# Optimization experiments

Hardware: AMD Instinct MI355X
Metric: run time of the kernel (lower is better)

## Reference

```python
import jax, jax.numpy as jnp
import numpy as np
import math

B, S, D, H = 4, 2048, 1024, 16
DH = D // H  # 64

def setup_inputs() -> dict:
    key = jax.random.key(0)
    ks = jax.random.split(key, 6)
    return {
        "x": jax.random.normal(ks[0], (B, S, D), dtype=jnp.float32),
        "alibi": jax.random.normal(ks[1], (1, H, S, S), dtype=jnp.float32),
        "w_qkv": jax.random.normal(ks[2], (3 * D, D), dtype=jnp.float32) * 0.02,
        "b_qkv": jax.random.normal(ks[3], (3 * D,), dtype=jnp.float32) * 0.02,
        "w_o": jax.random.normal(ks[4], (D, D), dtype=jnp.float32) * 0.02,
        "b_o": jax.random.normal(ks[5], (D,), dtype=jnp.float32) * 0.02,
    }

def reference(x, alibi, w_qkv, b_qkv, w_o, b_o):
    b, s, d = x.shape
    # torch Linear: y = x @ W.T + b
    qkv = x @ w_qkv.T + b_qkv                       # [B, S, 3D]
    qkv = qkv.reshape(b, s, H, 3, DH)               # interleaved per-head q,k,v
    q = jnp.swapaxes(qkv[:, :, :, 0, :], 1, 2)      # [B, H, S, DH]
    k = jnp.swapaxes(qkv[:, :, :, 1, :], 1, 2)
    v = jnp.swapaxes(qkv[:, :, :, 2, :], 1, 2)
    scores = jnp.einsum("bhqd,bhkd->bhqk", q, k) / math.sqrt(DH)
    attn = jax.nn.softmax(scores + alibi, axis=-1)  # [B, H, S, S]
    o = jnp.einsum("bhqk,bhkd->bhqd", attn, v)      # [B, H, S, DH]
    o = jnp.swapaxes(o, 1, 2).reshape(b, s, d)      # [B, S, D]
    return o @ w_o.T + b_o
```

## Files before the change

kernel.cpp:

```cpp
#include <hip/hip_runtime.h>
#include <stdint.h>

#define S_LEN 2048
#define NH    16
#define NB    4
#define DH    64
#define DMODEL 1024

using bf16x8 = __attribute__((ext_vector_type(8))) __bf16;
using f32x4  = __attribute__((ext_vector_type(4))) float;
using us8    = __attribute__((ext_vector_type(8))) unsigned short;

__device__ __forceinline__ unsigned short f2bf_rne(float f) {
    unsigned u = __builtin_bit_cast(unsigned, f);
    return (unsigned short)((u + 0x7FFFu + ((u >> 16) & 1u)) >> 16);
}

__device__ __forceinline__ bf16x8 ld_bf8(const unsigned short* p) {
    return __builtin_bit_cast(bf16x8, *(const us8*)p);
}

__device__ __forceinline__ f32x4 mfma16(bf16x8 a, bf16x8 b, f32x4 c) {
    return __builtin_amdgcn_mfma_f32_16x16x32_bf16(a, b, c, 0, 0, 0);
}

__device__ __forceinline__ float fast_exp2(float x) {
#if __has_builtin(__builtin_amdgcn_exp2f)
    return __builtin_amdgcn_exp2f(x);
#else
    return __expf(x * 0.69314718056f);
#endif
}

typedef __attribute__((address_space(1))) void* gp1_t;
typedef __attribute__((address_space(3))) void* lp3_t;

__device__ __forceinline__ void gload_lds16(const void* g, void* l) {
    __builtin_amdgcn_global_load_lds((gp1_t)(const_cast<void*>(g)), (lp3_t)l, 16, 0, 0);
}

__global__ void cvt_bf16(const float* __restrict__ in, unsigned short* __restrict__ out, int n4) {
    int i = blockIdx.x * 256 + threadIdx.x;
    if (i < n4) {
        float4 v = ((const float4*)in)[i];
        ushort4 o;
        o.x = f2bf_rne(v.x); o.y = f2bf_rne(v.y);
        o.z = f2bf_rne(v.z); o.w = f2bf_rne(v.w);
        ((ushort4*)out)[i] = o;
    }
}

template <int EPI>
__global__ __launch_bounds__(256) void gemm128(
    const unsigned short* __restrict__ A,
    const unsigned short* __restrict__ W,
    const float* __restrict__ bias,
    float* __restrict__ outF,
    unsigned short* __restrict__ Qb,
    unsigned short* __restrict__ Kb,
    unsigned short* __restrict__ Vt,
    int nTilesN)
{
    __shared__ __align__(16) unsigned short As[128 * 32];
    __shared__ __align__(16) unsigned short Bs[128 * 32];

    const int bm = blockIdx.x / nTilesN;
    const int bn = blockIdx.x % nTilesN;
    const int tileM = bm * 128, tileN = bn * 128;
    const int tid = threadIdx.x, lane = tid & 63, w = tid >> 6;
    const int m16 = lane & 15, quad = lane >> 4;
    const int wm = w >> 1, wn = w & 1;

    f32x4 acc[4][4] = {};

    const int c0 = w * 64 + lane;
    const int r0 = c0 >> 2, k0 = (c0 & 3) * 8;
    const int c1 = (4 + w) * 64 + lane;
    const int r1 = c1 >> 2, k1 = (c1 & 3) * 8;

    const unsigned short* Ag0 = A + (size_t)(tileM + r0) * 1024 + k0;
    const unsigned short* Ag1 = A + (size_t)(tileM + r1) * 1024 + k1;
    const unsigned short* Bg0 = W + (size_t)(tileN + r0) * 1024 + k0;
    const unsigned short* Bg1 = W + (size_t)(tileN + r1) * 1024 + k1;
    unsigned short* lA0 = &As[w * 512];
    unsigned short* lA1 = &As[(4 + w) * 512];
    unsigned short* lB0 = &Bs[w * 512];
    unsigned short* lB1 = &Bs[(4 + w) * 512];

    for (int kk = 0; kk < 1024; kk += 32) {
        gload_lds16(Ag0 + kk, lA0);
        gload_lds16(Ag1 + kk, lA1);
        gload_lds16(Bg0 + kk, lB0);
        gload_lds16(Bg1 + kk, lB1);
        __syncthreads();

        bf16x8 af[4], bf[4];
#pragma unroll
        for (int i = 0; i < 4; i++)
            af[i] = ld_bf8(&As[(wm * 64 + i * 16 + m16) * 32 + quad * 8]);
#pragma unroll
        for (int j = 0; j < 4; j++)
            bf[j] = ld_bf8(&Bs[(wn * 64 + j * 16 + m16) * 32 + quad * 8]);
#pragma unroll
        for (int i = 0; i < 4; i++)
#pragma unroll
            for (int j = 0; j < 4; j++)
                acc[i][j] = mfma16(af[i], bf[j], acc[i][j]);
        __syncthreads();
    }

#pragma unroll
    for (int i = 0; i < 4; i++) {
        const int mrow = tileM + wm * 64 + i * 16 + quad * 4;
#pragma unroll
        for (int j = 0; j < 4; j++) {
            const int nb0 = tileN + wn * 64 + j * 16;
            const int n = nb0 + m16;
            const float bv = bias[n];
            if (EPI == 0) {
                const int hh = nb0 / 192, rem = nb0 % 192;
                const int t = rem / 64, dbase = rem % 64;
                const int d = dbase + m16;
#pragma unroll
                for (int r = 0; r < 4; r++) {
                    float val = acc[i][j][r] + bv;
                    const int m = mrow + r;
                    const int b_ = m >> 11, s_ = m & 2047;
                    const size_t bh = (size_t)b_ * NH + hh;
                    if (t == 0)
                        Qb[(bh * S_LEN + s_) * DH + d] = f2bf_rne(val * 0.18033688f);
                    else if (t == 1)
                        Kb[(bh * S_LEN + s_) * DH + d] = f2bf_rne(val);
                    else
                        Vt[(bh * DH + d) * S_LEN + s_] = f2bf_rne(val);
                }
            } else {
#pragma unroll
                for (int r = 0; r < 4; r++) {
                    const int m = mrow + r;
                    outF[(size_t)m * DMODEL + n] = acc[i][j][r] + bv;
                }
            }
        }
    }
}

__global__ __launch_bounds__(256, 4) void attn(const unsigned short* __restrict__ Qb,
                                               const unsigned short* __restrict__ Kb,
                                               const unsigned short* __restrict__ Vt,
                                               const float* __restrict__ alibi,
                                               unsigned short* __restrict__ ob) {
    const int blk = blockIdx.x;
    const int xcd = blk & 7;
    const int b_  = (blk >> 3) & 3;
    const int hq  = xcd * 32 + (blk >> 5);
    const int hh  = hq >> 4, qt = hq & 15;
    const int tid = threadIdx.x, lane = tid & 63, w = tid >> 6;
    const int m16 = lane & 15, quad = lane >> 4;
    const int q0 = qt * 128;
    const size_t bh = (size_t)b_ * NH + hh;

    const unsigned short* Qp = Qb + (bh * S_LEN) * DH;
    const unsigned short* Kp = Kb + bh * S_LEN * DH;
    const unsigned short* Vp = Vt + bh * DH * S_LEN;

    __shared__ __align__(16) unsigned short Ks[128 * 64];
    __shared__ __align__(16) unsigned short Vs[64 * 128];
    __shared__ __align__(16) unsigned int   Pl[4][16 * 20];

    bf16x8 qfrag[2][2];
#pragma unroll
    for (int qf = 0; qf < 2; qf++) {
        const unsigned short* qp = Qp + (size_t)(q0 + w * 32 + qf * 16 + m16) * DH + quad * 8;
        qfrag[qf][0] = ld_bf8(qp);
        qfrag[qf][1] = ld_bf8(qp + 32);
    }
    const float* Apq[2];
#pragma unroll
    for (int qf = 0; qf < 2; qf++)
        Apq[qf] = alibi + ((size_t)hh * S_LEN + q0 + w * 32 + qf * 16 + m16) * S_LEN + quad * 4;

    int offk[4], offv[4];
#pragma unroll
    for (int t = 0; t < 4; t++) {
        const int ck = (w * 4 + t) * 64 + lane;
        const int rk = ck >> 3;
        offk[t] = rk * DH + ((ck & 7) ^ (rk & 7)) * 8;
        const int cv = ck;
        const int dv = cv >> 4;
        offv[t] = dv * S_LEN + ((cv & 15) ^ (dv & 15)) * 8;
    }

    const bf16x8 onesf = __builtin_bit_cast(bf16x8, (us8)(0x3F80u));
    f32x4 oacc[2][4] = {};
    f32x4 ssum[2] = {};
    unsigned int* plw = &Pl[w][0];
    const int sA = m16 & 7;

    for (int kc = 0; kc < S_LEN; kc += 128) {
        __syncthreads();
#pragma unroll
        for (int t = 0; t < 4; t++)
            gload_lds16(Kp + (size_t)kc * DH + offk[t], &Ks[(w * 4 + t) * 512]);
#pragma unroll
        for (int t = 0; t < 4; t++)
            gload_lds16(Vp + kc + offv[t], &Vs[(w * 4 + t) * 512]);
        __syncthreads();

#pragma unroll
        for (int qf = 0; qf < 2; qf++) {
            const bf16x8 qa = qfrag[qf][0], qb2 = qfrag[qf][1];
#pragma unroll
            for (int kc2 = 0; kc2 < 4; kc2++) {
                f32x4 sc[2];
#pragma unroll
                for (int t = 0; t < 2; t++) {
                    const int krow = (kc2 * 2 + t) * 16 + m16;
                    f32x4 z = {};
                    z = mfma16(ld_bf8(&Ks[krow * DH + (quad ^ sA) * 8]), qa, z);
                    z = mfma16(ld_bf8(&Ks[krow * DH + ((quad + 4) ^ sA) * 8]), qb2, z);
                    sc[t] = z;
                }
#pragma unroll
                for (int t = 0; t < 2; t++) {
                    const float4 al = *(const float4*)(Apq[qf] + kc + kc2 * 32 + t * 16);
                    float p0 = fast_exp2(__builtin_fmaf(al.x, 1.44269504f, sc[t][0]));
                    float p1 = fast_exp2(__builtin_fmaf(al.y, 1.44269504f, sc[t][1]));
                    float p2 = fast_exp2(__builtin_fmaf(al.z, 1.44269504f, sc[t][2]));
                    float p3 = fast_exp2(__builtin_fmaf(al.w, 1.44269504f, sc[t][3]));
                    uint2 pk;
                    pk.x = (__builtin_bit_cast(unsigned, p0) >> 16) |
                           (__builtin_bit_cast(unsigned, p1) & 0xFFFF0000u);
                    pk.y = (__builtin_bit_cast(unsigned, p2) >> 16) |
                           (__builtin_bit_cast(unsigned, p3) & 0xFFFF0000u);
                    *(uint2*)&plw[m16 * 20 + t * 8 + quad * 2] = pk;
                }
                const bf16x8 pf = ld_bf8((const unsigned short*)&plw[m16 * 20 + quad * 4]);
                ssum[qf] = mfma16(pf, onesf, ssum[qf]);
#pragma unroll
                for (int db = 0; db < 4; db++) {
                    const int vrow = db * 16 + m16;
                    const bf16x8 vf = ld_bf8(&Vs[vrow * 128 + ((kc2 * 4 + quad) ^ m16) * 8]);
                    oacc[qf][db] = mfma16(pf, vf, oacc[qf][db]);
                }
            }
        }
    }

#pragma unroll
    for (int qf = 0; qf < 2; qf++) {
        f32x4 rinv;
#pragma unroll
        for (int r = 0; r < 4; r++) rinv[r] = 1.0f / ssum[qf][r];
#pragma unroll
        for (int db = 0; db < 4; db++)
#pragma unroll
            for (int r = 0; r < 4; r++) {
                const int q = q0 + w * 32 + qf * 16 + quad * 4 + r;
                ob[((size_t)b_ * S_LEN + q) * DMODEL + hh * DH + db * 16 + m16] =
                    f2bf_rne(oacc[qf][db][r] * rinv[r]);
            }
    }
}

extern "C" void kernel_launch(void* const* d_in, const int* in_sizes, int n_in,
                              void* d_out, int out_size, void* d_ws, size_t ws_size,
                              hipStream_t stream) {
    (void)in_sizes; (void)n_in; (void)out_size; (void)ws_size;
    const float* x      = (const float*)d_in[0];
    const float* alibi  = (const float*)d_in[1];
    const float* w_qkv  = (const float*)d_in[2];
    const float* b_qkv  = (const float*)d_in[3];
    const float* w_o    = (const float*)d_in[4];
    const float* b_o    = (const float*)d_in[5];
    float* out = (float*)d_out;

    char* ws = (char*)d_ws;
    unsigned short* xb    = (unsigned short*)(ws);
    unsigned short* wqkvb = (unsigned short*)(ws + 16777216);
    unsigned short* wob   = (unsigned short*)(ws + 23068672);
    unsigned short* Qb    = (unsigned short*)(ws + 25165824);
    unsigned short* Kb    = (unsigned short*)(ws + 41943040);
    unsigned short* Vt    = (unsigned short*)(ws + 58720256);
    unsigned short* ob    = (unsigned short*)(ws + 75497472);

    cvt_bf16<<<8192, 256, 0, stream>>>(x, xb, 8388608 / 4);
    cvt_bf16<<<3072, 256, 0, stream>>>(w_qkv, wqkvb, 3145728 / 4);
    cvt_bf16<<<1024, 256, 0, stream>>>(w_o, wob, 1048576 / 4);

    gemm128<0><<<64 * 24, 256, 0, stream>>>(xb, wqkvb, b_qkv, nullptr, Qb, Kb, Vt, 24);
    attn<<<1024, 256, 0, stream>>>(Qb, Kb, Vt, alibi, ob);
    gemm128<1><<<64 * 8, 256, 0, stream>>>(ob, wob, b_o, out, nullptr, nullptr, nullptr, 8);
}
```

Before: 649.0 us.

## Rewrite attention inner loop with 32x32x16 MFMA and register-shuffled P

```diff
diff --git a/kernel.cpp b/kernel.cpp
--- a/kernel.cpp
+++ b/kernel.cpp
@@ -9,6 +9,7 @@
 
 using bf16x8 = __attribute__((ext_vector_type(8))) __bf16;
 using f32x4  = __attribute__((ext_vector_type(4))) float;
+using f32x16 = __attribute__((ext_vector_type(16))) float;
 using us8    = __attribute__((ext_vector_type(8))) unsigned short;
 
 __device__ __forceinline__ unsigned short f2bf_rne(float f) {
@@ -22,6 +23,10 @@
 
 __device__ __forceinline__ f32x4 mfma16(bf16x8 a, bf16x8 b, f32x4 c) {
     return __builtin_amdgcn_mfma_f32_16x16x32_bf16(a, b, c, 0, 0, 0);
+}
+
+__device__ __forceinline__ f32x16 mfma32(bf16x8 a, bf16x8 b, f32x16 c) {
+    return __builtin_amdgcn_mfma_f32_32x32x16_bf16(a, b, c, 0, 0, 0);
 }
 
 __device__ __forceinline__ float fast_exp2(float x) {
@@ -121,18 +126,23 @@
                 const int hh = nb0 / 192, rem = nb0 % 192;
                 const int t = rem / 64, dbase = rem % 64;
                 const int d = dbase + m16;
-#pragma unroll
-                for (int r = 0; r < 4; r++) {
-                    float val = acc[i][j][r] + bv;
-                    const int m = mrow + r;
-                    const int b_ = m >> 11, s_ = m & 2047;
-                    const size_t bh = (size_t)b_ * NH + hh;
-                    if (t == 0)
-                        Qb[(bh * S_LEN + s_) * DH + d] = f2bf_rne(val * 0.18033688f);
-                    else if (t == 1)
-                        Kb[(bh * S_LEN + s_) * DH + d] = f2bf_rne(val);
-                    else
-                        Vt[(bh * DH + d) * S_LEN + s_] = f2bf_rne(val);
+                const int b_ = mrow >> 11, s0 = mrow & 2047;
+                const size_t bh = (size_t)b_ * NH + hh;
+                if (t == 2) {
+                    ushort4 pk;
+                    pk.x = f2bf_rne(acc[i][j][0] + bv);
+                    pk.y = f2bf_rne(acc[i][j][1] + bv);
+                    pk.z = f2bf_rne(acc[i][j][2] + bv);
+                    pk.w = f2bf_rne(acc[i][j][3] + bv);
+                    *(ushort4*)&Vt[(bh * DH + d) * S_LEN + s0] = pk;
+                } else {
+#pragma unroll
+                    for (int r = 0; r < 4; r++) {
+                        float val = acc[i][j][r] + bv;
+                        const size_t idx = (bh * S_LEN + s0 + r) * DH + d;
+                        if (t == 0) Qb[idx] = f2bf_rne(val * 0.18033688f);
+                        else        Kb[idx] = f2bf_rne(val);
+                    }
                 }
             } else {
 #pragma unroll
@@ -151,116 +161,119 @@
                                                const float* __restrict__ alibi,
                                                unsigned short* __restrict__ ob) {
     const int blk = blockIdx.x;
-    const int xcd = blk & 7;
-    const int b_  = (blk >> 3) & 3;
-    const int hq  = xcd * 32 + (blk >> 5);
-    const int hh  = hq >> 4, qt = hq & 15;
+    const int xcd   = blk & 7;
+    const int inner = blk >> 3;
+    const int hh = (inner & 1) * 8 + xcd;
+    const int b_ = (inner >> 1) & 3;
+    const int qt = inner >> 3;
     const int tid = threadIdx.x, lane = tid & 63, w = tid >> 6;
-    const int m16 = lane & 15, quad = lane >> 4;
+    const int l31 = lane & 31, h = lane >> 5;
     const int q0 = qt * 128;
     const size_t bh = (size_t)b_ * NH + hh;
 
-    const unsigned short* Qp = Qb + (bh * S_LEN) * DH;
     const unsigned short* Kp = Kb + bh * S_LEN * DH;
     const unsigned short* Vp = Vt + bh * DH * S_LEN;
 
     __shared__ __align__(16) unsigned short Ks[128 * 64];
     __shared__ __align__(16) unsigned short Vs[64 * 128];
-    __shared__ __align__(16) unsigned int   Pl[4][16 * 20];
-
-    bf16x8 qfrag[2][2];
-#pragma unroll
-    for (int qf = 0; qf < 2; qf++) {
-        const unsigned short* qp = Qp + (size_t)(q0 + w * 32 + qf * 16 + m16) * DH + quad * 8;
-        qfrag[qf][0] = ld_bf8(qp);
-        qfrag[qf][1] = ld_bf8(qp + 32);
-    }
-    const float* Apq[2];
-#pragma unroll
-    for (int qf = 0; qf < 2; qf++)
-        Apq[qf] = alibi + ((size_t)hh * S_LEN + q0 + w * 32 + qf * 16 + m16) * S_LEN + quad * 4;
-
-    int offk[4], offv[4];
-#pragma unroll
-    for (int t = 0; t < 4; t++) {
-        const int ck = (w * 4 + t) * 64 + lane;
-        const int rk = ck >> 3;
-        offk[t] = rk * DH + ((ck & 7) ^ (rk & 7)) * 8;
-        const int cv = ck;
-        const int dv = cv >> 4;
-        offv[t] = dv * S_LEN + ((cv & 15) ^ (dv & 15)) * 8;
-    }
-
-    const bf16x8 onesf = __builtin_bit_cast(bf16x8, (us8)(0x3F80u));
-    f32x4 oacc[2][4] = {};
-    f32x4 ssum[2] = {};
-    unsigned int* plw = &Pl[w][0];
-    const int sA = m16 & 7;
+
+    const int qrow = q0 + w * 32 + l31;
+    bf16x8 qfrag[4];
+#pragma unroll
+    for (int kd = 0; kd < 4; kd++)
+        qfrag[kd] = ld_bf8(Qb + (bh * S_LEN + qrow) * DH + kd * 16 + h * 8);
+
+    const float* Ap = alibi + ((size_t)hh * S_LEN + qrow) * S_LEN + h * 4;
+
+    int koff[4], voff[4];
+#pragma unroll
+    for (int i = 0; i < 4; i++) {
+        const int u = i * 256 + w * 64 + lane;
+        const int kr = u >> 3, kc_ = u & 7;
+        koff[i] = kr * DH + (kc_ ^ (kr & 7)) * 8;
+        const int vd = u >> 4, vc = u & 15;
+        voff[i] = vd * S_LEN + (vc ^ (vd & 15)) * 8;
+    }
+
+    f32x16 oacc[2] = {};
+    float ssum = 0.0f;
 
     for (int kc = 0; kc < S_LEN; kc += 128) {
         __syncthreads();
 #pragma unroll
-        for (int t = 0; t < 4; t++)
-            gload_lds16(Kp + (size_t)kc * DH + offk[t], &Ks[(w * 4 + t) * 512]);
-#pragma unroll
-        for (int t = 0; t < 4; t++)
-            gload_lds16(Vp + kc + offv[t], &Vs[(w * 4 + t) * 512]);
+        for (int i = 0; i < 4; i++)
+            gload_lds16(Kp + (size_t)kc * DH + koff[i], &Ks[(i * 256 + w * 64) * 8]);
+#pragma unroll
+        for (int i = 0; i < 4; i++)
+            gload_lds16(Vp + kc + voff[i], &Vs[(i * 256 + w * 64) * 8]);
         __syncthreads();
 
 #pragma unroll
-        for (int qf = 0; qf < 2; qf++) {
-            const bf16x8 qa = qfrag[qf][0], qb2 = qfrag[qf][1];
-#pragma unroll
-            for (int kc2 = 0; kc2 < 4; kc2++) {
-                f32x4 sc[2];
-#pragma unroll
-                for (int t = 0; t < 2; t++) {
-                    const int krow = (kc2 * 2 + t) * 16 + m16;
-                    f32x4 z = {};
-                    z = mfma16(ld_bf8(&Ks[krow * DH + (quad ^ sA) * 8]), qa, z);
-                    z = mfma16(ld_bf8(&Ks[krow * DH + ((quad + 4) ^ sA) * 8]), qb2, z);
-                    sc[t] = z;
-                }
-#pragma unroll
-                for (int t = 0; t < 2; t++) {
-                    const float4 al = *(const float4*)(Apq[qf] + kc + kc2 * 32 + t * 16);
-                    float p0 = fast_exp2(__builtin_fmaf(al.x, 1.44269504f, sc[t][0]));
-                    float p1 = fast_exp2(__builtin_fmaf(al.y, 1.44269504f, sc[t][1]));
-                    float p2 = fast_exp2(__builtin_fmaf(al.z, 1.44269504f, sc[t][2]));
-                    float p3 = fast_exp2(__builtin_fmaf(al.w, 1.44269504f, sc[t][3]));
-                    uint2 pk;
-                    pk.x = (__builtin_bit_cast(unsigned, p0) >> 16) |
-                           (__builtin_bit_cast(unsigned, p1) & 0xFFFF0000u);
-                    pk.y = (__builtin_bit_cast(unsigned, p2) >> 16) |
-                           (__builtin_bit_cast(unsigned, p3) & 0xFFFF0000u);
-                    *(uint2*)&plw[m16 * 20 + t * 8 + quad * 2] = pk;
-                }
-                const bf16x8 pf = ld_bf8((const unsigned short*)&plw[m16 * 20 + quad * 4]);
-                ssum[qf] = mfma16(pf, onesf, ssum[qf]);
-#pragma unroll
-                for (int db = 0; db < 4; db++) {
-                    const int vrow = db * 16 + m16;
-                    const bf16x8 vf = ld_bf8(&Vs[vrow * 128 + ((kc2 * 4 + quad) ^ m16) * 8]);
-                    oacc[qf][db] = mfma16(pf, vf, oacc[qf][db]);
-                }
+        for (int kt = 0; kt < 4; kt++) {
+            f32x16 sacc = {};
+#pragma unroll
+            for (int kd = 0; kd < 4; kd++) {
+                const bf16x8 kf =
+                    ld_bf8(&Ks[(kt * 32 + l31) * DH + (((kd * 2 + h) ^ (l31 & 7)) * 8)]);
+                sacc = mfma32(kf, qfrag[kd], sacc);
+            }
+            unsigned Sd[8];
+#pragma unroll
+            for (int g = 0; g < 4; g++) {
+                const float4 al = *(const float4*)(Ap + kc + kt * 32 + g * 8);
+                unsigned u0 = __builtin_bit_cast(unsigned,
+                    fast_exp2(__builtin_fmaf(al.x, 1.44269504f, sacc[4 * g + 0]))) & 0xFFFF0000u;
+                unsigned u1 = __builtin_bit_cast(unsigned,
+                    fast_exp2(__builtin_fmaf(al.y, 1.44269504f, sacc[4 * g + 1]))) & 0xFFFF0000u;
+                unsigned u2 = __builtin_bit_cast(unsigned,
+                    fast_exp2(__builtin_fmaf(al.z, 1.44269504f, sacc[4 * g + 2]))) & 0xFFFF0000u;
+                unsigned u3 = __builtin_bit_cast(unsigned,
+                    fast_exp2(__builtin_fmaf(al.w, 1.44269504f, sacc[4 * g + 3]))) & 0xFFFF0000u;
+                ssum += (__builtin_bit_cast(float, u0) + __builtin_bit_cast(float, u1)) +
+                        (__builtin_bit_cast(float, u2) + __builtin_bit_cast(float, u3));
+                Sd[2 * g]     = (u0 >> 16) | u1;
+                Sd[2 * g + 1] = (u2 >> 16) | u3;
+            }
+            const unsigned r0 = (unsigned)__shfl_xor((int)(h ? Sd[0] : Sd[2]), 32);
+            const unsigned r1 = (unsigned)__shfl_xor((int)(h ? Sd[1] : Sd[3]), 32);
+            const unsigned r2 = (unsigned)__shfl_xor((int)(h ? Sd[4] : Sd[6]), 32);
+            const unsigned r3 = (unsigned)__shfl_xor((int)(h ? Sd[5] : Sd[7]), 32);
+            uint4 f1, f2;
+            if (h == 0) {
+                f1 = make_uint4(Sd[0], Sd[1], r0, r1);
+                f2 = make_uint4(Sd[4], Sd[5], r2, r3);
+            } else {
+                f1 = make_uint4(r0, r1, Sd[2], Sd[3]);
+                f2 = make_uint4(r2, r3, Sd[6], Sd[7]);
+            }
+            const bf16x8 pf1 = __builtin_bit_cast(bf16x8, f1);
+            const bf16x8 pf2 = __builtin_bit_cast(bf16x8, f2);
+#pragma unroll
+            for (int dblk = 0; dblk < 2; dblk++) {
+                const bf16x8 vf1 = ld_bf8(
+                    &Vs[(dblk * 32 + l31) * 128 + (((kt * 4 + h) ^ (l31 & 15)) * 8)]);
+                oacc[dblk] = mfma32(vf1, pf1, oacc[dblk]);
+                const bf16x8 vf2 = ld_bf8(
+                    &Vs[(dblk * 32 + l31) * 128 + (((kt * 4 + 2 + h) ^ (l31 & 15)) * 8)]);
+                oacc[dblk] = mfma32(vf2, pf2, oacc[dblk]);
             }
         }
     }
 
-#pragma unroll
-    for (int qf = 0; qf < 2; qf++) {
-        f32x4 rinv;
-#pragma unroll
-        for (int r = 0; r < 4; r++) rinv[r] = 1.0f / ssum[qf][r];
-#pragma unroll
-        for (int db = 0; db < 4; db++)
-#pragma unroll
-            for (int r = 0; r < 4; r++) {
-                const int q = q0 + w * 32 + qf * 16 + quad * 4 + r;
-                ob[((size_t)b_ * S_LEN + q) * DMODEL + hh * DH + db * 16 + m16] =
-                    f2bf_rne(oacc[qf][db][r] * rinv[r]);
-            }
-    }
+    const float tot = ssum + __shfl_xor(ssum, 32);
+    const float rinv = 1.0f / tot;
+    unsigned short* orow = ob + ((size_t)b_ * S_LEN + qrow) * DMODEL + hh * DH;
+#pragma unroll
+    for (int dblk = 0; dblk < 2; dblk++)
+#pragma unroll
+        for (int rg = 0; rg < 4; rg++) {
+            ushort4 pk;
+            pk.x = f2bf_rne(oacc[dblk][4 * rg + 0] * rinv);
+            pk.y = f2bf_rne(oacc[dblk][4 * rg + 1] * rinv);
+            pk.z = f2bf_rne(oacc[dblk][4 * rg + 2] * rinv);
+            pk.w = f2bf_rne(oacc[dblk][4 * rg + 3] * rinv);
+            *(ushort4*)(orow + dblk * 32 + rg * 8 + h * 4) = pk;
+        }
 }
 
 extern "C" void kernel_launch(void* const* d_in, const int* in_sizes, int n_in,
```

New measurement: 653.2 us. About the same (+0.6%).
